# Performance work log

Measured on AMD Instinct MI355X. Metric: run time of the kernel, lower is better.

Reference implementation:

```python
import jax, jax.numpy as jnp
import numpy as np

N = 100000   # nodes
E = 3200000  # edges (avg degree 32)
IN = 128     # in_channels
H = 128      # hidden_channels
G = 512      # graphs in batch


def setup_inputs() -> dict:
    key = jax.random.key(0)
    ks = jax.random.split(key, 8)
    x = jax.random.normal(ks[0], (N, IN), dtype=jnp.float32)
    edge_index = jax.random.randint(ks[1], (2, E), 0, N, dtype=jnp.int64)
    batch = jnp.sort(jax.random.randint(ks[2], (N,), 0, G, dtype=jnp.int64))
    s_in = 1.0 / np.sqrt(IN)
    s_h = 1.0 / np.sqrt(H)
    W1 = jax.random.normal(ks[3], (IN, H), dtype=jnp.float32) * s_in
    b1 = jnp.zeros((H,), dtype=jnp.float32)
    W2 = jax.random.normal(ks[4], (H, H), dtype=jnp.float32) * s_h
    b2 = jnp.zeros((H,), dtype=jnp.float32)
    Wc = jax.random.normal(ks[5], (H, 1), dtype=jnp.float32) * s_h
    bc = jnp.zeros((1,), dtype=jnp.float32)
    return {"x": x, "edge_index": edge_index, "batch": batch,
            "W1": W1, "b1": b1, "W2": W2, "b2": b2, "Wc": Wc, "bc": bc}


def _gcn_conv(x, W, b, src, dst, n):
    # PyG GCNConv: x' = D^{-1/2} (A+I) D^{-1/2} X W + b  (self-loops already in src/dst)
    h = x @ W                                      # [n, H] small GEMM
    ones = jnp.ones(src.shape[0], dtype=h.dtype)
    deg = jax.ops.segment_sum(ones, dst, num_segments=n)
    dinv = jnp.where(deg > 0, jax.lax.rsqrt(deg), 0.0)
    norm = dinv[src] * dinv[dst]                   # [E+n]
    msgs = h[src] * norm[:, None]                  # gather + scale (memory-bound)
    return jax.ops.segment_sum(msgs, dst, num_segments=n) + b


def reference(x, edge_index, batch, W1, b1, W2, b2, Wc, bc):
    n = x.shape[0]
    loop = jnp.arange(n, dtype=edge_index.dtype)
    src = jnp.concatenate([edge_index[0], loop])   # add self-loops
    dst = jnp.concatenate([edge_index[1], loop])
    h = jax.nn.relu(_gcn_conv(x, W1, b1, src, dst, n))
    h = jax.nn.relu(_gcn_conv(h, W2, b2, src, dst, n))
    # global_mean_pool: segment mean over graph ids
    counts = jax.ops.segment_sum(jnp.ones(n, dtype=h.dtype), batch, num_segments=G)
    sums = jax.ops.segment_sum(h, batch, num_segments=G)
    pooled = sums / jnp.maximum(counts, 1.0)[:, None]   # [G, H]
    return jax.nn.sigmoid(pooled @ Wc + bc)             # [G, 1]
```

## Files before the change

kernel.cpp:

```cpp
#include <hip/hip_runtime.h>

typedef unsigned short ushort_t;
typedef unsigned int uint_t;
typedef unsigned char u8_t;

typedef __bf16 bf16x8 __attribute__((ext_vector_type(8)));
typedef float f32x4 __attribute__((ext_vector_type(4)));
typedef uint_t uint32x4 __attribute__((ext_vector_type(4)));
typedef uint_t uint32x2 __attribute__((ext_vector_type(2)));
typedef _Float16 h2 __attribute__((ext_vector_type(2)));

#define EPB 20480
#define NSH 7
#define CAP 6144
#define BPAD 1032

__device__ __forceinline__ float b2f(ushort_t u) {
    union { uint_t ui; float f; } c; c.ui = ((uint_t)u) << 16; return c.f;
}
__device__ __forceinline__ ushort_t f2b(float f) {
    union { float f; uint_t ui; } c; c.f = f;
    uint_t u = c.ui;
    uint_t r = (u + 0x7fffu + ((u >> 16) & 1u)) >> 16;
    return (ushort_t)r;
}
__device__ __forceinline__ u8_t f2e5(float x) {
    ushort_t h = __builtin_bit_cast(ushort_t, (_Float16)x);
    uint_t r = ((uint_t)h + 0x7Fu + ((h >> 8) & 1u)) >> 8;
    return (u8_t)r;
}
__device__ __forceinline__ void upk_add(uint_t d, h2* acc) {
    uint_t A = __builtin_amdgcn_perm(0u, d, 0x010C000Cu);
    uint_t B = __builtin_amdgcn_perm(0u, d, 0x030C020Cu);
    acc[0] += __builtin_bit_cast(h2, A);
    acc[1] += __builtin_bit_cast(h2, B);
}

__global__ __launch_bounds__(256) void p1_hist(const int* __restrict__ dst,
                                               int* __restrict__ H,
                                               const float* __restrict__ W1,
                                               const float* __restrict__ W2,
                                               ushort_t* __restrict__ W1t,
                                               ushort_t* __restrict__ W2t,
                                               u8_t* __restrict__ h8z,
                                               int E, int NBLK, int B, int N) {
    int t = threadIdx.x, c = blockIdx.x;
    if (c >= NBLK + 128) {
        if (t < 32) ((uint_t*)h8z)[(size_t)N * 32 + t] = 0u;
        return;
    }
    if (c >= NBLK) {
        int idx = (c - NBLK) * 256 + t;
        int sel = idx >> 14;
        int i = idx & 16383;
        int k = i >> 7, nn = i & 127;
        const float* S = sel ? W2 : W1;
        ushort_t* D = sel ? W2t : W1t;
        D[nn * 128 + k] = f2b(S[k * 128 + nn]);
        return;
    }
    __shared__ int hist[1024];
    for (int b = t; b < 1024; b += 256) hist[b] = 0;
    __syncthreads();
    int base = c * EPB;
    int lim = min(E - base, EPB);
    for (int i = t; i < lim; i += 256)
        atomicAdd(&hist[dst[base + i] >> NSH], 1);
    __syncthreads();
    for (int b = t; b < B; b += 256) H[b * NBLK + c] = hist[b];
}

__global__ __launch_bounds__(256) void reduce256(const int* __restrict__ in,
                                                 int* __restrict__ bsums, int n) {
    __shared__ int s[256];
    int t = threadIdx.x, g = blockIdx.x * 256 + t;
    s[t] = (g < n) ? in[g] : 0;
    __syncthreads();
    for (int o = 128; o > 0; o >>= 1) {
        if (t < o) s[t] += s[t + o];
        __syncthreads();
    }
    if (t == 0) bsums[blockIdx.x] = s[0];
}

__global__ __launch_bounds__(512) void scan_small(const int* __restrict__ in,
                                                  int* __restrict__ outEx, int n) {
    __shared__ int s[512];
    int t = threadIdx.x;
    int v = (t < n) ? in[t] : 0;
    s[t] = v;
    __syncthreads();
    for (int o = 1; o < 512; o <<= 1) {
        int x = 0;
        if (t >= o) x = s[t - o];
        __syncthreads();
        s[t] += x;
        __syncthreads();
    }
    if (t < n) outEx[t] = s[t] - v;
}

__global__ __launch_bounds__(256) void scan256ex(const int* __restrict__ in,
                                                 const int* __restrict__ boffs,
                                                 int* __restrict__ outEx, int n) {
    __shared__ int s[256];
    int t = threadIdx.x, g = blockIdx.x * 256 + t;
    int v = (g < n) ? in[g] : 0;
    s[t] = v;
    __syncthreads();
    for (int o = 1; o < 256; o <<= 1) {
        int x = 0;
        if (t >= o) x = s[t - o];
        __syncthreads();
        s[t] += x;
        __syncthreads();
    }
    if (g < n) outEx[g] = boffs[blockIdx.x] + s[t] - v;
}

__global__ __launch_bounds__(256) void p3_scatter(const int* __restrict__ src,
                                                  const int* __restrict__ dst,
                                                  const int* __restrict__ Hex,
                                                  uint_t* __restrict__ packed,
                                                  int E, int NBLK, int B) {
    __shared__ int offsL[1024];
    __shared__ int cur[1024];
    int t = threadIdx.x, c = blockIdx.x;
    for (int b = t; b < B; b += 256) {
        offsL[b] = Hex[b * NBLK + c];
        cur[b] = 0;
    }
    __syncthreads();
    int base = c * EPB;
    int lim = min(E - base, EPB);
    for (int i = t; i < lim; i += 256) {
        int d = dst[base + i];
        int s = src[base + i];
        int b = d >> NSH;
        int r = atomicAdd(&cur[b], 1);
        packed[offsL[b] + r] = ((uint_t)s << NSH) | (uint_t)(d & 127);
    }
}

__global__ __launch_bounds__(256) void p4_build(const uint_t* __restrict__ packed,
                                                const int* __restrict__ Hex,
                                                int* __restrict__ adj,
                                                int* __restrict__ offs,
                                                int* __restrict__ dgr,
                                                float* __restrict__ dinv,
                                                int E, int N, int NBLK, int B) {
    __shared__ uint_t ebuf[CAP];
    __shared__ int dcnt[128], loc[128], cur[128];
    __shared__ int pdg[128], ploc[128];
    int t = threadIdx.x, b = blockIdx.x;
    int bs = Hex[b * NBLK];
    int be = (b + 1 < B) ? Hex[(b + 1) * NBLK] : E;
    int m = be - bs;
    if (t < 128) dcnt[t] = 0;
    __syncthreads();
    bool fits = (m <= CAP);
    for (int i = t; i < m; i += 256) {
        uint_t p = packed[bs + i];
        if (fits) ebuf[i] = p;
        atomicAdd(&dcnt[p & 127], 1);
    }
    __syncthreads();
    if (t < 128) {
        int pd = (dcnt[t] + 8) & ~7;
        pdg[t] = pd;
        ploc[t] = pd;
    }
    __syncthreads();
    for (int o = 1; o < 128; o <<= 1) {
        int x = 0;
        if (t < 128 && t >= o) x = ploc[t - o];
        __syncthreads();
        if (t < 128) ploc[t] += x;
        __syncthreads();
    }
    int bsp = ((bs + 7) & ~7) + b * BPAD;
    if (t < 128) {
        int ex = ploc[t] - pdg[t];
        int node = b * 128 + t;
        if (node < N) {
            int nbase = bsp + ex;
            offs[node] = nbase;
            dgr[node]  = pdg[t];
            dinv[node] = rsqrtf((float)(dcnt[t] + 1));
            adj[nbase] = node;
            for (int i = dcnt[t] + 1; i < pdg[t]; ++i)
                adj[nbase + i] = N;
        }
        loc[t] = ex + 1;
        cur[t] = 0;
    }
    __syncthreads();
    if (fits) {
        for (int i = t; i < m; i += 256) {
            uint_t p = ebuf[i];
            int l = p & 127;
            int r = atomicAdd(&cur[l], 1);
            adj[bsp + loc[l] + r] = (int)(p >> NSH);
        }
    } else {
        for (int i = t; i < m; i += 256) {
            uint_t p = packed[bs + i];
            int l = p & 127;
            int r = atomicAdd(&cur[l], 1);
            adj[bsp + loc[l] + r] = (int)(p >> NSH);
        }
    }
}

__global__ __launch_bounds__(256, 4) void gemm_scale(const ushort_t* __restrict__ Xin,
                                                     const ushort_t* __restrict__ Wt,
                                                     const float* __restrict__ dinv,
                                                     u8_t* __restrict__ Hout8, int n) {
    __shared__ ushort_t lds[128 * 136];
    int tid = threadIdx.x;
    for (int i = tid; i < 128 * 16; i += 256) {
        int r = i >> 4, c8 = (i & 15) << 3;
        *(uint32x4*)(lds + r * 136 + c8) = *(const uint32x4*)(Wt + r * 128 + c8);
    }
    __syncthreads();
    int lane = tid & 63, wave = tid >> 6;
    int m = lane & 15, q = lane >> 4;
    int row0 = blockIdx.x * 64 + wave * 16;
    int ar = row0 + m;
    if (ar > n - 1) ar = n - 1;
    bf16x8 a[4];
#pragma unroll
    for (int ks = 0; ks < 4; ++ks)
        a[ks] = __builtin_bit_cast(bf16x8,
            *(const uint32x4*)(Xin + (size_t)ar * 128 + ks * 32 + q * 8));
    f32x4 acc[8];
    f32x4 zero = {0.f, 0.f, 0.f, 0.f};
#pragma unroll
    for (int nt = 0; nt < 8; ++nt) acc[nt] = zero;
#pragma unroll
    for (int nt = 0; nt < 8; ++nt) {
#pragma unroll
        for (int ks = 0; ks < 4; ++ks) {
            bf16x8 b = __builtin_bit_cast(bf16x8,
                *(const uint32x4*)(lds + (nt * 16 + m) * 136 + ks * 32 + q * 8));
            acc[nt] = __builtin_amdgcn_mfma_f32_16x16x32_bf16(a[ks], b, acc[nt], 0, 0, 0);
        }
    }
    float dv[4];
#pragma unroll
    for (int r = 0; r < 4; ++r) {
        int gr = row0 + q * 4 + r;
        dv[r] = (gr < n) ? dinv[gr] : 0.f;
    }
#pragma unroll
    for (int nt = 0; nt < 8; ++nt) {
#pragma unroll
        for (int r = 0; r < 4; ++r) {
            int gr = row0 + q * 4 + r;
            if (gr < n)
                Hout8[(size_t)gr * 128 + nt * 16 + m] = f2e5(acc[nt][r] * dv[r]);
        }
    }
}

__global__ __launch_bounds__(256, 4) void gemm_scale_f32(const float* __restrict__ Xf,
                                                         const ushort_t* __restrict__ Wt,
                                                         const float* __restrict__ dinv,
                                                         u8_t* __restrict__ Hout8, int n) {
    __shared__ ushort_t lds[128 * 136];
    int tid = threadIdx.x;
    for (int i = tid; i < 128 * 16; i += 256) {
        int r = i >> 4, c8 = (i & 15) << 3;
        *(uint32x4*)(lds + r * 136 + c8) = *(const uint32x4*)(Wt + r * 128 + c8);
    }
    __syncthreads();
    int lane = tid & 63, wave = tid >> 6;
    int m = lane & 15, q = lane >> 4;
    int row0 = blockIdx.x * 64 + wave * 16;
    int ar = row0 + m;
    if (ar > n - 1) ar = n - 1;
    bf16x8 a[4];
#pragma unroll
    for (int ks = 0; ks < 4; ++ks) {
        const float* p = Xf + (size_t)ar * 128 + ks * 32 + q * 8;
        f32x4 lo = *(const f32x4*)p;
        f32x4 hi = *(const f32x4*)(p + 4);
        ushort_t t[8];
        t[0] = f2b(lo[0]); t[1] = f2b(lo[1]); t[2] = f2b(lo[2]); t[3] = f2b(lo[3]);
        t[4] = f2b(hi[0]); t[5] = f2b(hi[1]); t[6] = f2b(hi[2]); t[7] = f2b(hi[3]);
        a[ks] = __builtin_bit_cast(bf16x8, *(uint32x4*)t);
    }
    f32x4 acc[8];
    f32x4 zero = {0.f, 0.f, 0.f, 0.f};
#pragma unroll
    for (int nt = 0; nt < 8; ++nt) acc[nt] = zero;
#pragma unroll
    for (int nt = 0; nt < 8; ++nt) {
#pragma unroll
        for (int ks = 0; ks < 4; ++ks) {
            bf16x8 b = __builtin_bit_cast(bf16x8,
                *(const uint32x4*)(lds + (nt * 16 + m) * 136 + ks * 32 + q * 8));
            acc[nt] = __builtin_amdgcn_mfma_f32_16x16x32_bf16(a[ks], b, acc[nt], 0, 0, 0);
        }
    }
    float dv[4];
#pragma unroll
    for (int r = 0; r < 4; ++r) {
        int gr = row0 + q * 4 + r;
        dv[r] = (gr < n) ? dinv[gr] : 0.f;
    }
#pragma unroll
    for (int nt = 0; nt < 8; ++nt) {
#pragma unroll
        for (int r = 0; r < 4; ++r) {
            int gr = row0 + q * 4 + r;
            if (gr < n)
                Hout8[(size_t)gr * 128 + nt * 16 + m] = f2e5(acc[nt][r] * dv[r]);
        }
    }
}

__device__ __forceinline__ void agg_core(const u8_t* __restrict__ Hs8,
                                         const int* __restrict__ adj,
                                         int beg, int pd, int g, uint_t colb,
                                         h2* acc) {
    int e = 0;
    for (; e + 16 <= pd; e += 16) {
        const int4 sv = *(const int4*)(adj + beg + e + g * 4);
        uint_t o0 = ((uint_t)sv.x << 7) | colb;
        uint_t o1 = ((uint_t)sv.y << 7) | colb;
        uint_t o2 = ((uint_t)sv.z << 7) | colb;
        uint_t o3 = ((uint_t)sv.w << 7) | colb;
        uint32x2 w0 = *(const uint32x2*)(Hs8 + o0);
        uint32x2 w1 = *(const uint32x2*)(Hs8 + o1);
        uint32x2 w2 = *(const uint32x2*)(Hs8 + o2);
        uint32x2 w3 = *(const uint32x2*)(Hs8 + o3);
        upk_add(w0[0], acc); upk_add(w0[1], acc + 2);
        upk_add(w1[0], acc); upk_add(w1[1], acc + 2);
        upk_add(w2[0], acc); upk_add(w2[1], acc + 2);
        upk_add(w3[0], acc); upk_add(w3[1], acc + 2);
    }
    if (e < pd) {
        const int2 sv = *(const int2*)(adj + beg + e + g * 2);
        uint_t o0 = ((uint_t)sv.x << 7) | colb;
        uint_t o1 = ((uint_t)sv.y << 7) | colb;
        uint32x2 w0 = *(const uint32x2*)(Hs8 + o0);
        uint32x2 w1 = *(const uint32x2*)(Hs8 + o1);
        upk_add(w0[0], acc); upk_add(w0[1], acc + 2);
        upk_add(w1[0], acc); upk_add(w1[1], acc + 2);
    }
}

__device__ __forceinline__ void slot_reduce(h2* acc) {
#pragma unroll
    for (int k = 0; k < 4; ++k) {
        uint_t v = __builtin_bit_cast(uint_t, acc[k]);
        acc[k] += __builtin_bit_cast(h2, (uint_t)__shfl_xor(v, 16, 64));
        v = __builtin_bit_cast(uint_t, acc[k]);
        acc[k] += __builtin_bit_cast(h2, (uint_t)__shfl_xor(v, 32, 64));
    }
}

__global__ __launch_bounds__(256, 4) void agg_kernel(const u8_t* __restrict__ Hs8,
                                                     const int* __restrict__ adj,
                                                     const int* __restrict__ offs,
                                                     const int* __restrict__ dgr,
                                                     const float* __restrict__ dinv,
                                                     const float* __restrict__ bias,
                                                     ushort_t* __restrict__ Out, int n) {
    int node = blockIdx.x * 4 + (threadIdx.x >> 6);
    if (node >= n) return;
    int lane = threadIdx.x & 63;
    int g = lane >> 4;
    int l16 = lane & 15;
    uint_t colb = (uint_t)l16 * 8;
    const int beg = offs[node];
    const int pd  = dgr[node];
    h2 acc[4];
    h2 hz = {(_Float16)0.f, (_Float16)0.f};
#pragma unroll
    for (int k = 0; k < 4; ++k) acc[k] = hz;
    agg_core(Hs8, adj, beg, pd, g, colb, acc);
    slot_reduce(acc);
    if (g == 0) {
        float di = dinv[node];
        ushort_t o[8];
#pragma unroll
        for (int k = 0; k < 4; ++k) {
            float f0 = (float)acc[k][0];
            float f1 = (float)acc[k][1];
            o[2 * k]     = f2b(fmaxf(di * f0 + bias[colb + 2 * k], 0.f));
            o[2 * k + 1] = f2b(fmaxf(di * f1 + bias[colb + 2 * k + 1], 0.f));
        }
        *(uint32x4*)(Out + (size_t)node * 128 + colb) = *(uint32x4*)o;
    }
}

__global__ __launch_bounds__(256, 4) void agg_pool_kernel(const u8_t* __restrict__ Hs8,
                                                          const int* __restrict__ adj,
                                                          const int* __restrict__ offs,
                                                          const int* __restrict__ dgr,
                                                          const float* __restrict__ dinv,
                                                          const float* __restrict__ bias,
                                                          const float* __restrict__ Wc,
                                                          float* __restrict__ Sout, int n) {
    int node = blockIdx.x * 4 + (threadIdx.x >> 6);
    if (node >= n) return;
    int lane = threadIdx.x & 63;
    int g = lane >> 4;
    int l16 = lane & 15;
    uint_t colb = (uint_t)l16 * 8;
    const int beg = offs[node];
    const int pd  = dgr[node];
    h2 acc[4];
    h2 hz = {(_Float16)0.f, (_Float16)0.f};
#pragma unroll
    for (int k = 0; k < 4; ++k) acc[k] = hz;
    agg_core(Hs8, adj, beg, pd, g, colb, acc);
    slot_reduce(acc);
    float local = 0.f;
    float di = dinv[node];
#pragma unroll
    for (int k = 0; k < 4; ++k) {
        float f0 = fmaxf(di * (float)acc[k][0] + bias[colb + 2 * k], 0.f);
        float f1 = fmaxf(di * (float)acc[k][1] + bias[colb + 2 * k + 1], 0.f);
        local += f0 * Wc[colb + 2 * k] + f1 * Wc[colb + 2 * k + 1];
    }
    local += __shfl_xor(local, 1, 64);
    local += __shfl_xor(local, 2, 64);
    local += __shfl_xor(local, 4, 64);
    local += __shfl_xor(local, 8, 64);
    if (lane == 0) Sout[node] = local;
}

__global__ __launch_bounds__(256) void pool2_kernel(const float* __restrict__ S,
                                                    const int* __restrict__ batch,
                                                    const float* __restrict__ bc,
                                                    float* __restrict__ out, int n) {
    int g = blockIdx.x;
    int t = threadIdx.x;
    int lo = 0, hi = n;
    while (lo < hi) { int mid = (lo + hi) >> 1; if (batch[mid] < g) lo = mid + 1; else hi = mid; }
    int start = lo;
    hi = n;
    while (lo < hi) { int mid = (lo + hi) >> 1; if (batch[mid] < g + 1) lo = mid + 1; else hi = mid; }
    int stop = lo;
    float s = 0.f;
    for (int i = start + t; i < stop; i += 256) s += S[i];
    __shared__ float red[256];
    red[t] = s;
    __syncthreads();
    for (int o = 128; o > 0; o >>= 1) {
        if (t < o) red[t] += red[t + o];
        __syncthreads();
    }
    if (t == 0) {
        int cg = stop - start;
        float z = red[0] / (float)(cg > 0 ? cg : 1) + bc[0];
        out[g] = 1.f / (1.f + expf(-z));
    }
}

extern "C" void kernel_launch(void* const* d_in, const int* in_sizes, int n_in,
                              void* d_out, int out_size, void* d_ws, size_t ws_size,
                              hipStream_t stream) {
    const float* X     = (const float*)d_in[0];
    const int* ei      = (const int*)d_in[1];
    const int* batch   = (const int*)d_in[2];
    const float* W1    = (const float*)d_in[3];
    const float* b1    = (const float*)d_in[4];
    const float* W2    = (const float*)d_in[5];
    const float* b2    = (const float*)d_in[6];
    const float* Wc    = (const float*)d_in[7];
    const float* bc    = (const float*)d_in[8];

    const int N = in_sizes[2];
    const int E = in_sizes[1] / 2;
    const int G = out_size;
    const int* srcv = ei;
    const int* dstv = ei + E;

    const int NBLK = (E + EPB - 1) / EPB;
    const int B    = (N + 127) >> NSH;
    const int n0   = B * NBLK;
    const int g1   = (n0 + 255) / 256;

    char* p = (char*)d_ws;
    auto alloc = [&](size_t bytes) -> void* {
        void* r = (void*)p;
        p += (bytes + 255) & ~(size_t)255;
        return r;
    };
    int* H         = (int*)alloc((size_t)n0 * 4);
    int* Hex       = (int*)alloc((size_t)n0 * 4);
    int* S1        = (int*)alloc((size_t)g1 * 4);
    int* S1ex      = (int*)alloc((size_t)g1 * 4);
    uint_t* packed = (uint_t*)alloc((size_t)E * 4);
    int* adj       = (int*)alloc(((size_t)E + (size_t)B * BPAD + 128) * 4);
    int* offs      = (int*)alloc(((size_t)N + 1) * 4);
    int* dgr       = (int*)alloc((size_t)N * 4);
    float* dinv    = (float*)alloc((size_t)N * 4);
    ushort_t* W1t  = (ushort_t*)alloc(16384 * 2);
    ushort_t* W2t  = (ushort_t*)alloc(16384 * 2);
    u8_t* h8       = (u8_t*)alloc(((size_t)N + 1) * 128);
    ushort_t* bufA = (ushort_t*)alloc((size_t)N * 128 * 2);
    float* Snode   = (float*)alloc((size_t)N * 4);

    p1_hist<<<NBLK + 129, 256, 0, stream>>>(dstv, H, W1, W2, W1t, W2t, h8, E, NBLK, B, N);
    reduce256<<<g1, 256, 0, stream>>>(H, S1, n0);
    scan_small<<<1, 512, 0, stream>>>(S1, S1ex, g1);
    scan256ex<<<g1, 256, 0, stream>>>(H, S1ex, Hex, n0);
    p3_scatter<<<NBLK, 256, 0, stream>>>(srcv, dstv, Hex, packed, E, NBLK, B);
    p4_build<<<B, 256, 0, stream>>>(packed, Hex, adj, offs, dgr, dinv, E, N, NBLK, B);

    const int GB = (N + 63) / 64;
    const int AB = (N + 3) / 4;
    gemm_scale_f32<<<GB, 256, 0, stream>>>(X, W1t, dinv, h8, N);
    agg_kernel<<<AB, 256, 0, stream>>>(h8, adj, offs, dgr, dinv, b1, bufA, N);
    gemm_scale<<<GB, 256, 0, stream>>>(bufA, W2t, dinv, h8, N);
    agg_pool_kernel<<<AB, 256, 0, stream>>>(h8, adj, offs, dgr, dinv, b2, Wc, Snode, N);
    pool2_kernel<<<G, 256, 0, stream>>>(Snode, batch, bc, (float*)d_out, N);
}
```

Before: 378.7 us.

## Widen CSR build buckets to 512 nodes and shrink edge chunks

Changes the two-pass bucketed CSR construction to group destinations into 512-node buckets, with smaller per-block edge chunks for histogram and scatter. p4_build now runs 512 threads per bucket and drops the LDS edge cache, so it reads packed edges from global memory twice. The aim is to rebalance block counts and bucket sizes across the build kernels. The risk is fewer, heavier p4 blocks than there are CUs, plus the extra global reads.

```diff
diff --git a/kernel.cpp b/kernel.cpp
--- a/kernel.cpp
+++ b/kernel.cpp
@@ -10,10 +10,10 @@
 typedef uint_t uint32x2 __attribute__((ext_vector_type(2)));
 typedef _Float16 h2 __attribute__((ext_vector_type(2)));
 
-#define EPB 20480
-#define NSH 7
-#define CAP 6144
-#define BPAD 1032
+#define EPB 5120
+#define NSH 9
+#define MSK 511
+#define BPAD 4104
 
 __device__ __forceinline__ float b2f(ushort_t u) {
     union { uint_t ui; float f; } c; c.ui = ((uint_t)u) << 16; return c.f;
@@ -59,15 +59,15 @@
         D[nn * 128 + k] = f2b(S[k * 128 + nn]);
         return;
     }
-    __shared__ int hist[1024];
-    for (int b = t; b < 1024; b += 256) hist[b] = 0;
+    __shared__ int hist[256];
+    if (t < 256) hist[t] = 0;
     __syncthreads();
     int base = c * EPB;
     int lim = min(E - base, EPB);
     for (int i = t; i < lim; i += 256)
         atomicAdd(&hist[dst[base + i] >> NSH], 1);
     __syncthreads();
-    for (int b = t; b < B; b += 256) H[b * NBLK + c] = hist[b];
+    if (t < B) H[t * NBLK + c] = hist[t];
 }
 
 __global__ __launch_bounds__(256) void reduce256(const int* __restrict__ in,
@@ -123,12 +123,12 @@
                                                   const int* __restrict__ Hex,
                                                   uint_t* __restrict__ packed,
                                                   int E, int NBLK, int B) {
-    __shared__ int offsL[1024];
-    __shared__ int cur[1024];
+    __shared__ int offsL[256];
+    __shared__ int cur[256];
     int t = threadIdx.x, c = blockIdx.x;
-    for (int b = t; b < B; b += 256) {
-        offsL[b] = Hex[b * NBLK + c];
-        cur[b] = 0;
+    if (t < B) {
+        offsL[t] = Hex[t * NBLK + c];
+        cur[t] = 0;
     }
     __syncthreads();
     int base = c * EPB;
@@ -138,77 +138,58 @@
         int s = src[base + i];
         int b = d >> NSH;
         int r = atomicAdd(&cur[b], 1);
-        packed[offsL[b] + r] = ((uint_t)s << NSH) | (uint_t)(d & 127);
-    }
-}
-
-__global__ __launch_bounds__(256) void p4_build(const uint_t* __restrict__ packed,
+        packed[offsL[b] + r] = ((uint_t)s << NSH) | (uint_t)(d & MSK);
+    }
+}
+
+__global__ __launch_bounds__(512) void p4_build(const uint_t* __restrict__ packed,
                                                 const int* __restrict__ Hex,
                                                 int* __restrict__ adj,
                                                 int* __restrict__ offs,
                                                 int* __restrict__ dgr,
                                                 float* __restrict__ dinv,
                                                 int E, int N, int NBLK, int B) {
-    __shared__ uint_t ebuf[CAP];
-    __shared__ int dcnt[128], loc[128], cur[128];
-    __shared__ int pdg[128], ploc[128];
+    __shared__ int dcnt[512], loc[512], cur[512], sps[512];
     int t = threadIdx.x, b = blockIdx.x;
     int bs = Hex[b * NBLK];
     int be = (b + 1 < B) ? Hex[(b + 1) * NBLK] : E;
     int m = be - bs;
-    if (t < 128) dcnt[t] = 0;
-    __syncthreads();
-    bool fits = (m <= CAP);
-    for (int i = t; i < m; i += 256) {
+    dcnt[t] = 0;
+    __syncthreads();
+    for (int i = t; i < m; i += 512)
+        atomicAdd(&dcnt[packed[bs + i] & MSK], 1);
+    __syncthreads();
+    int d = dcnt[t];
+    int pd = (d + 8) & ~7;
+    sps[t] = pd;
+    __syncthreads();
+    for (int o = 1; o < 512; o <<= 1) {
+        int x = 0;
+        if (t >= o) x = sps[t - o];
+        __syncthreads();
+        sps[t] += x;
+        __syncthreads();
+    }
+    int bsp = ((bs + 7) & ~7) + b * BPAD;
+    int ex = sps[t] - pd;
+    int node = b * 512 + t;
+    if (node < N) {
+        int nbase = bsp + ex;
+        offs[node] = nbase;
+        dgr[node]  = pd;
+        dinv[node] = rsqrtf((float)(d + 1));
+        adj[nbase] = node;
+        for (int i = d + 1; i < pd; ++i)
+            adj[nbase + i] = N;
+    }
+    loc[t] = ex + 1;
+    cur[t] = 0;
+    __syncthreads();
+    for (int i = t; i < m; i += 512) {
         uint_t p = packed[bs + i];
-        if (fits) ebuf[i] = p;
-        atomicAdd(&dcnt[p & 127], 1);
-    }
-    __syncthreads();
-    if (t < 128) {
-        int pd = (dcnt[t] + 8) & ~7;
-        pdg[t] = pd;
-        ploc[t] = pd;
-    }
-    __syncthreads();
-    for (int o = 1; o < 128; o <<= 1) {
-        int x = 0;
-        if (t < 128 && t >= o) x = ploc[t - o];
-        __syncthreads();
-        if (t < 128) ploc[t] += x;
-        __syncthreads();
-    }
-    int bsp = ((bs + 7) & ~7) + b * BPAD;
-    if (t < 128) {
-        int ex = ploc[t] - pdg[t];
-        int node = b * 128 + t;
-        if (node < N) {
-            int nbase = bsp + ex;
-            offs[node] = nbase;
-            dgr[node]  = pdg[t];
-            dinv[node] = rsqrtf((float)(dcnt[t] + 1));
-            adj[nbase] = node;
-            for (int i = dcnt[t] + 1; i < pdg[t]; ++i)
-                adj[nbase + i] = N;
-        }
-        loc[t] = ex + 1;
-        cur[t] = 0;
-    }
-    __syncthreads();
-    if (fits) {
-        for (int i = t; i < m; i += 256) {
-            uint_t p = ebuf[i];
-            int l = p & 127;
-            int r = atomicAdd(&cur[l], 1);
-            adj[bsp + loc[l] + r] = (int)(p >> NSH);
-        }
-    } else {
-        for (int i = t; i < m; i += 256) {
-            uint_t p = packed[bs + i];
-            int l = p & 127;
-            int r = atomicAdd(&cur[l], 1);
-            adj[bsp + loc[l] + r] = (int)(p >> NSH);
-        }
+        int l = p & MSK;
+        int r = atomicAdd(&cur[l], 1);
+        adj[bsp + loc[l] + r] = (int)(p >> NSH);
     }
 }
 
@@ -481,7 +462,7 @@
     const int* dstv = ei + E;
 
     const int NBLK = (E + EPB - 1) / EPB;
-    const int B    = (N + 127) >> NSH;
+    const int B    = (N + MSK) >> NSH;
     const int n0   = B * NBLK;
     const int g1   = (n0 + 255) / 256;
 
@@ -496,7 +477,7 @@
     int* S1        = (int*)alloc((size_t)g1 * 4);
     int* S1ex      = (int*)alloc((size_t)g1 * 4);
     uint_t* packed = (uint_t*)alloc((size_t)E * 4);
-    int* adj       = (int*)alloc(((size_t)E + (size_t)B * BPAD + 128) * 4);
+    int* adj       = (int*)alloc(((size_t)E + (size_t)B * BPAD + 4224) * 4);
     int* offs      = (int*)alloc(((size_t)N + 1) * 4);
     int* dgr       = (int*)alloc((size_t)N * 4);
     float* dinv    = (float*)alloc((size_t)N * 4);
@@ -511,7 +492,7 @@
     scan_small<<<1, 512, 0, stream>>>(S1, S1ex, g1);
     scan256ex<<<g1, 256, 0, stream>>>(H, S1ex, Hex, n0);
     p3_scatter<<<NBLK, 256, 0, stream>>>(srcv, dstv, Hex, packed, E, NBLK, B);
-    p4_build<<<B, 256, 0, stream>>>(packed, Hex, adj, offs, dgr, dinv, E, N, NBLK, B);
+    p4_build<<<B, 512, 0, stream>>>(packed, Hex, adj, offs, dgr, dinv, E, N, NBLK, B);
 
     const int GB = (N + 63) / 64;
     const int AB = (N + 3) / 4;
```

After: 339.6 us. -10.3%, faster.
